# Optimization experiments

Measured on AMD Instinct MI355X. Metric: run time of the kernel, lower is better.

Reference implementation:

```python
import jax, jax.numpy as jnp
import numpy as np

N_HEADS = 32
N_KV_HEADS = 8
HEAD_DIM = 128
DIM = 4096
ROPE_THETA = 500000.0
BSZ, SEQLEN = 4, 1024


def _rope(t, cos, sin):
    # t: [B,S,H,hd]; cos/sin: [S,hd//2]
    te = t[..., 0::2]
    to = t[..., 1::2]
    c = cos[None, :, None, :]
    s = sin[None, :, None, :]
    out = jnp.stack([te * c - to * s, te * s + to * c], axis=-1)
    return out.reshape(t.shape)


def setup_inputs() -> dict:
    key = jax.random.key(0)
    ks = jax.random.split(key, 8)
    scale = 1.0 / np.sqrt(DIM)
    x = jax.random.normal(ks[0], (BSZ, SEQLEN, DIM), dtype=jnp.float32)
    wq = jax.random.normal(ks[1], (DIM, N_HEADS * HEAD_DIM), dtype=jnp.float32) * scale
    wk = jax.random.normal(ks[2], (DIM, N_KV_HEADS * HEAD_DIM), dtype=jnp.float32) * scale
    wv = jax.random.normal(ks[3], (DIM, N_KV_HEADS * HEAD_DIM), dtype=jnp.float32) * scale
    wo = jax.random.normal(ks[4], (N_HEADS * HEAD_DIM, DIM), dtype=jnp.float32) * scale
    # rotary tables: freqs_cis[s, j] = exp(i * s * theta^(-2j/hd))
    inv_freq = 1.0 / (ROPE_THETA ** (np.arange(0, HEAD_DIM, 2, dtype=np.float32) / HEAD_DIM))
    ang = np.outer(np.arange(SEQLEN, dtype=np.float32), inv_freq)
    freqs_cos = jnp.asarray(np.cos(ang), dtype=jnp.float32)
    freqs_sin = jnp.asarray(np.sin(ang), dtype=jnp.float32)
    # additive causal mask: 0 on/below diag, -inf above
    causal_mask = jnp.triu(jnp.full((SEQLEN, SEQLEN), -jnp.inf, dtype=jnp.float32), k=1)
    return {"x": x, "wq": wq, "wk": wk, "wv": wv, "wo": wo,
            "freqs_cos": freqs_cos, "freqs_sin": freqs_sin,
            "causal_mask": causal_mask, "fixed_point_iter": 0, "start_pos": 0}


def reference(x, wq, wk, wv, wo, freqs_cos, freqs_sin, causal_mask, fixed_point_iter, start_pos):
    B, S, _ = x.shape
    n_rep = N_HEADS // N_KV_HEADS
    xq = (x @ wq).reshape(B, S, N_HEADS, HEAD_DIM)
    xk = (x @ wk).reshape(B, S, N_KV_HEADS, HEAD_DIM)
    xv = (x @ wv).reshape(B, S, N_KV_HEADS, HEAD_DIM)
    xq = _rope(xq, freqs_cos, freqs_sin)
    xk = _rope(xk, freqs_cos, freqs_sin)
    # start_pos == 0 prefill: cache slice [:start_pos+S] equals freshly written xk/xv
    keys = jnp.repeat(xk, n_rep, axis=2)    # [B,S,H,hd]
    values = jnp.repeat(xv, n_rep, axis=2)
    scores = jnp.einsum('bqhd,bkhd->bhqk', xq, keys) / np.sqrt(HEAD_DIM)
    scores = scores + causal_mask  # broadcast [S,S]
    probs = jax.nn.softmax(scores.astype(jnp.float32), axis=-1).astype(xq.dtype)
    out = jnp.einsum('bhqk,bkhd->bqhd', probs, values)
    out = out.reshape(B, S, N_HEADS * HEAD_DIM)
    return out @ wo
```

## Files before the change

### kernel.cpp

```cpp
#include <hip/hip_runtime.h>

#define BSZ_  4
#define SEQ_  1024
#define NH_   32
#define NKVH_ 8
#define HD_   128
#define DIM_  4096
#define NTOK_ (BSZ_ * SEQ_)
#define QKVW_ 6144

typedef float  floatx4  __attribute__((ext_vector_type(4)));
typedef float  floatx16 __attribute__((ext_vector_type(16)));
typedef __bf16 bf16x8   __attribute__((ext_vector_type(8)));
typedef unsigned short ushortx8 __attribute__((ext_vector_type(8)));

__device__ __forceinline__ float fast_exp2(float x) {
  return __builtin_amdgcn_exp2f(x);
}

__device__ __forceinline__ unsigned short f2bf_bits(float f) {
  unsigned int u = __float_as_uint(f);
  u += 0x7FFFu + ((u >> 16) & 1u);
  return (unsigned short)(u >> 16);
}
__device__ __forceinline__ unsigned int pack_bf2_rne(float lo, float hi_) {
  return (unsigned int)f2bf_bits(lo) | ((unsigned int)f2bf_bits(hi_) << 16);
}
__device__ __forceinline__ unsigned int pack_bf2_trunc(float lo, float hi_) {
  return __builtin_amdgcn_perm(__float_as_uint(hi_), __float_as_uint(lo), 0x07060302u);
}

__device__ __forceinline__ void gld16(const void* g, void* l) {
  __builtin_amdgcn_global_load_lds(
      (const __attribute__((address_space(1))) void*)g,
      (__attribute__((address_space(3))) void*)l, 16, 0, 0);
}

__global__ __launch_bounds__(256)
void xconv(const float* __restrict__ X, unsigned short* __restrict__ XB)
{
  size_t i = ((size_t)blockIdx.x * 256 + threadIdx.x) * 4;
  float4 v = *(const float4*)&X[i];
  ushort4 o;
  o.x = f2bf_bits(v.x); o.y = f2bf_bits(v.y);
  o.z = f2bf_bits(v.z); o.w = f2bf_bits(v.w);
  *(ushort4*)&XB[i] = o;
}

__global__ __launch_bounds__(256)
void wtrans(const float* __restrict__ W, unsigned short* __restrict__ WT,
            int K, int N)
{
  __shared__ unsigned short T[32][36];
  const int k0 = blockIdx.y * 32, n0 = blockIdx.x * 32;
  const int t = threadIdx.x;
  {
    int kr = t >> 3, nc = (t & 7) * 4;
    float4 v = *(const float4*)&W[(size_t)(k0 + kr) * N + n0 + nc];
    T[kr][nc + 0] = f2bf_bits(v.x);
    T[kr][nc + 1] = f2bf_bits(v.y);
    T[kr][nc + 2] = f2bf_bits(v.z);
    T[kr][nc + 3] = f2bf_bits(v.w);
  }
  __syncthreads();
  {
    int nr = t >> 3, kc = (t & 7) * 4;
    ushort4 o;
    o.x = T[kc + 0][nr]; o.y = T[kc + 1][nr];
    o.z = T[kc + 2][nr]; o.w = T[kc + 3][nr];
    *(ushort4*)&WT[(size_t)(n0 + nr) * K + k0 + kc] = o;
  }
}

__global__ __launch_bounds__(256)
void vtrans2(const unsigned short* __restrict__ qkv, unsigned short* __restrict__ VT)
{
  __shared__ unsigned short T[32][36];
  const int bh = blockIdx.z;
  const int s0 = blockIdx.x * 32, d0 = blockIdx.y * 32;
  const int b = bh >> 3, kvh = bh & 7;
  const int t = threadIdx.x;
  {
    int sr = t >> 3, dc = (t & 7) * 4;
    ushort4 v = *(const ushort4*)&qkv[(size_t)(b * SEQ_ + s0 + sr) * QKVW_ + 5120 + kvh * HD_ + d0 + dc];
    T[sr][dc + 0] = v.x; T[sr][dc + 1] = v.y;
    T[sr][dc + 2] = v.z; T[sr][dc + 3] = v.w;
  }
  __syncthreads();
  {
    int dr = t >> 3, sc = (t & 7) * 4;
    ushort4 o;
    o.x = T[sc + 0][dr]; o.y = T[sc + 1][dr];
    o.z = T[sc + 2][dr]; o.w = T[sc + 3][dr];
    *(ushort4*)&VT[((size_t)bh * HD_ + d0 + dr) * SEQ_ + s0 + sc] = o;
  }
}

__global__ __launch_bounds__(256)
void rope2(unsigned int* __restrict__ t, const float* __restrict__ cosf,
           const float* __restrict__ sinf, int shift, int stride_u32, int base_u32)
{
  int idx = blockIdx.x * 256 + threadIdx.x;
  int tok = idx >> shift;
  int rem = idx & ((1 << shift) - 1);
  int d2  = idx & 63;
  int pos = tok & (SEQ_ - 1);
  unsigned int* p = &t[(size_t)tok * stride_u32 + base_u32 + rem];
  unsigned int pv = *p;
  float xe = __uint_as_float(pv << 16);
  float xo = __uint_as_float(pv & 0xFFFF0000u);
  float cv = cosf[pos * 64 + d2];
  float sv = sinf[pos * 64 + d2];
  float oe = xe * cv - xo * sv;
  float oo = xe * sv + xo * cv;
  *p = pack_bf2_rne(oe, oo);
}

template<bool OUT_BF16>
__global__ __launch_bounds__(512, 2)
void gemm_v4(const unsigned short* __restrict__ A,
             const unsigned short* __restrict__ B,
             void* __restrict__ Cout, int M, int N, int K)
{
  __shared__ __align__(16) unsigned short As[4][256][32];
  __shared__ __align__(16) unsigned short Bs[4][256][32];

  const int tid  = threadIdx.x;
  const int w    = tid >> 6;
  const int lane = tid & 63;
  const int l16  = lane & 15;
  const int quad = lane >> 4;
  const int wr   = w >> 2;
  const int wc   = w & 3;

  int wg = blockIdx.x;
  const int q8 = gridDim.x >> 3;
  wg = (wg & 7) * q8 + (wg >> 3);
  const int nbx = N >> 8;
  const int bm = (wg / nbx) * 256;
  const int bn = (wg % nbx) * 256;

  const int srow = w * 16 + (lane >> 2);
  const int scs  = (lane & 3) ^ ((srow >> 1) & 3);
  const unsigned short* Ag = &A[(size_t)(bm + srow) * K + scs * 8];
  const unsigned short* Bg = &B[(size_t)(bn + srow) * K + scs * 8];
  const size_t half = (size_t)128 * K;
  char* AsW = (char*)&As[0][0][0] + w * 1024;
  char* BsW = (char*)&Bs[0][0][0] + w * 1024;

  const int ntiles = K >> 5;

  auto stage = [&](int kt, int buf) {
    size_t ko = (size_t)kt << 5;
    gld16(Ag + ko,        AsW + buf * 16384);
    gld16(Ag + ko + half, AsW + buf * 16384 + 8192);
    gld16(Bg + ko,        BsW + buf * 16384);
    gld16(Bg + ko + half, BsW + buf * 16384 + 8192);
  };

  floatx4 acc[8][4];
#pragma unroll
  for (int i = 0; i < 8; i++)
#pragma unroll
    for (int j = 0; j < 4; j++) acc[i][j] = (floatx4){0.f, 0.f, 0.f, 0.f};

  const int cfr = quad ^ ((l16 >> 1) & 3);

  auto ldfrags = [&](int kt, bf16x8* aF, bf16x8* bF) {
    const int buf = kt & 3;
    const unsigned short* Ab = &As[buf][wr * 128 + l16][cfr * 8];
    const unsigned short* Bb = &Bs[buf][wc * 64  + l16][cfr * 8];
#pragma unroll
    for (int i = 0; i < 8; i++) aF[i] = *(const bf16x8*)&Ab[i * (16 * 32)];
#pragma unroll
    for (int j = 0; j < 4; j++) bF[j] = *(const bf16x8*)&Bb[j * (16 * 32)];
  };

  auto domfma = [&](bf16x8* aF, bf16x8* bF) {
    __builtin_amdgcn_s_setprio(1);
#pragma unroll
    for (int i = 0; i < 8; i++)
#pragma unroll
      for (int j = 0; j < 4; j++)
        acc[i][j] = __builtin_amdgcn_mfma_f32_16x16x32_bf16(aF[i], bF[j], acc[i][j], 0, 0, 0);
    __builtin_amdgcn_s_setprio(0);
  };

  auto syncstep = [&]() {
    asm volatile("s_waitcnt vmcnt(8)" ::: "memory");
    asm volatile("s_waitcnt lgkmcnt(0)" ::: "memory");
    __builtin_amdgcn_s_barrier();
    __builtin_amdgcn_sched_barrier(0);
  };

  bf16x8 aF0[8], bF0[4], aF1[8], bF1[4];

  stage(0, 0); stage(1, 1); stage(2, 2);
  syncstep();
  ldfrags(0, aF0, bF0);

#pragma unroll 1
  for (int t = 0; t < ntiles; t += 2) {
    {
      int pk = t + 3 < ntiles ? t + 3 : 0;
      stage(pk, (t + 3) & 3);
    }
    syncstep();
    ldfrags(t + 1, aF1, bF1);
    domfma(aF0, bF0);

    {
      int pk = t + 4 < ntiles ? t + 4 : 0;
      stage(pk, (t + 4) & 3);
    }
    syncstep();
    {
      int kt2 = t + 2 < ntiles ? t + 2 : 0;
      ldfrags(kt2, aF0, bF0);
    }
    domfma(aF1, bF1);
  }

  asm volatile("s_waitcnt vmcnt(0)" ::: "memory");

#pragma unroll
  for (int i = 0; i < 8; i++)
#pragma unroll
    for (int j = 0; j < 4; j++)
#pragma unroll
      for (int r = 0; r < 4; r++) {
        size_t row = bm + wr * 128 + i * 16 + quad * 4 + r;
        size_t col = bn + wc * 64 + j * 16 + l16;
        if (OUT_BF16)
          ((unsigned short*)Cout)[row * N + col] = f2bf_bits(acc[i][j][r]);
        else
          ((float*)Cout)[row * N + col] = acc[i][j][r];
      }
}

__global__ __launch_bounds__(256, 2)
void flash_attn2(const unsigned short* __restrict__ qkv,
                 const unsigned short* __restrict__ vt,
                 unsigned short* __restrict__ o)
{
  __shared__ __align__(16) unsigned short S_[4][8192];
  unsigned short* Ks = &S_[0][0];
  unsigned short* Vs = &S_[1][0];

  const int qt = blockIdx.x, h = blockIdx.y, b = blockIdx.z;
  const int kvh = h >> 2;
  const int tid = threadIdx.x, w = tid >> 6, lane = tid & 63;
  const int l31 = lane & 31, hi = lane >> 5;
  const int qb = qt * 256, qw = qb + w * 64;
  unsigned short* Ps = &S_[2][0] + w * 4096;

  const float CEXP = (float)(0.08838834764831845 * 1.4426950408889634);

  bf16x8 qf[2][8];
#pragma unroll
  for (int t2 = 0; t2 < 2; t2++) {
    const unsigned short* qrow =
        &qkv[(size_t)(b * SEQ_ + qw + t2 * 32 + l31) * QKVW_ + h * HD_ + hi * 8];
#pragma unroll
    for (int s = 0; s < 8; s++)
      qf[t2][s] = *(const bf16x8*)&qrow[s * 16];
  }

  floatx16 oa[2][4];
#pragma unroll
  for (int t2 = 0; t2 < 2; t2++)
#pragma unroll
    for (int dt = 0; dt < 4; dt++)
#pragma unroll
      for (int r = 0; r < 16; r++) oa[t2][dt][r] = 0.f;

  float ms[2] = {-3.0e38f, -3.0e38f};
  float ls[2] = {0.f, 0.f};

  const int nk = qb + 256;
  const int qmaxw = qw + 63;

  for (int kb_ = 0; kb_ < nk; kb_ += 64) {
    __syncthreads();
    {
      const size_t gbase = (size_t)(b * SEQ_ + kb_) * QKVW_ + 4096 + kvh * HD_;
#pragma unroll
      for (int it = 0; it < 4; it++) {
        int idx = it * 256 + tid;
        int key = idx >> 4, c = idx & 15;
        ushortx8 vld = *(const ushortx8*)&qkv[gbase + (size_t)key * QKVW_ + c * 8];
        *(ushortx8*)&Ks[key * 128 + ((c ^ (key & 15)) * 8)] = vld;
      }
      const size_t vbase = ((size_t)(b * NKVH_ + kvh) * HD_) * SEQ_ + kb_;
#pragma unroll
      for (int it = 0; it < 4; it++) {
        int idx = it * 256 + tid;
        int d = idx >> 3, c = idx & 7;
        ushortx8 vld = *(const ushortx8*)&vt[vbase + (size_t)d * SEQ_ + c * 8];
        *(ushortx8*)&Vs[d * 64 + ((c ^ (d & 7)) * 8)] = vld;
      }
    }
    __syncthreads();

    if (kb_ <= qmaxw) {
      const bool needmask = (kb_ + 63 > qw);

#pragma unroll
      for (int t2 = 0; t2 < 2; t2++) {
        floatx16 sc[2];
#pragma unroll
        for (int r = 0; r < 16; r++) { sc[0][r] = 0.f; sc[1][r] = 0.f; }
#pragma unroll
        for (int s = 0; s < 8; s++) {
          int c = 2 * s + hi;
          bf16x8 k0 = *(const bf16x8*)&Ks[l31 * 128 + ((c ^ (l31 & 15)) * 8)];
          bf16x8 k1 = *(const bf16x8*)&Ks[(32 + l31) * 128 + ((c ^ ((32 + l31) & 15)) * 8)];
          sc[0] = __builtin_amdgcn_mfma_f32_32x32x16_bf16(k0, qf[t2][s], sc[0], 0, 0, 0);
          sc[1] = __builtin_amdgcn_mfma_f32_32x32x16_bf16(k1, qf[t2][s], sc[1], 0, 0, 0);
        }

        if (needmask) {
          const int q = qw + t2 * 32 + l31;
#pragma unroll
          for (int k2 = 0; k2 < 2; k2++)
#pragma unroll
            for (int r = 0; r < 16; r++) {
              int key = kb_ + k2 * 32 + (r & 3) + 8 * (r >> 2) + 4 * hi;
              if (key > q) sc[k2][r] = -3.0e38f;
            }
        }

        float mx0 = sc[0][0], mx1 = sc[0][1];
#pragma unroll
        for (int r = 2; r < 16; r += 2) { mx0 = fmaxf(mx0, sc[0][r]); mx1 = fmaxf(mx1, sc[0][r + 1]); }
#pragma unroll
        for (int r = 0; r < 16; r += 2) { mx0 = fmaxf(mx0, sc[1][r]); mx1 = fmaxf(mx1, sc[1][r + 1]); }
        float mx = fmaxf(mx0, mx1);
        mx = fmaxf(mx, __shfl_xor(mx, 32));
        float mxs = mx * CEXP;
        float mn = fmaxf(ms[t2], mxs);
        float alpha = fast_exp2(ms[t2] - mn);
        ms[t2] = mn;

        float rs0 = 0.f, rs1 = 0.f;
        const int qloc = t2 * 32 + l31;
#pragma unroll
        for (int k2 = 0; k2 < 2; k2++) {
          unsigned int pk[8];
#pragma unroll
          for (int r = 0; r < 16; r += 2) {
            float p0 = fast_exp2(__builtin_fmaf(sc[k2][r],     CEXP, -mn));
            float p1 = fast_exp2(__builtin_fmaf(sc[k2][r + 1], CEXP, -mn));
            rs0 += p0; rs1 += p1;
            pk[r >> 1] = pack_bf2_trunc(p0, p1);
          }
#pragma unroll
          for (int rq = 0; rq < 4; rq++) {
            int keyoff = k2 * 32 + 8 * rq + 4 * hi;
            int c = keyoff >> 3;
            uint2 val = {pk[rq * 2], pk[rq * 2 + 1]};
            *(uint2*)&Ps[qloc * 64 + ((c ^ (qloc & 7)) * 8) + (keyoff & 7)] = val;
          }
        }
        float rs = rs0 + rs1;
        rs += __shfl_xor(rs, 32);
        ls[t2] = ls[t2] * alpha + rs;

        if (__any(alpha != 1.0f)) {
#pragma unroll
          for (int dt = 0; dt < 4; dt++)
#pragma unroll
            for (int r = 0; r < 16; r++) oa[t2][dt][r] *= alpha;
        }
      }

#pragma unroll
      for (int ks = 0; ks < 4; ks++) {
        int c = 2 * ks + hi;
        bf16x8 pf0, pf1;
        {
          int q0l = l31;
          int q1l = 32 + l31;
          pf0 = *(const bf16x8*)&Ps[q0l * 64 + ((c ^ (q0l & 7)) * 8)];
          pf1 = *(const bf16x8*)&Ps[q1l * 64 + ((c ^ (q1l & 7)) * 8)];
        }
#pragma unroll
        for (int dt = 0; dt < 4; dt++) {
          int d = dt * 32 + l31;
          bf16x8 vf = *(const bf16x8*)&Vs[d * 64 + ((c ^ (d & 7)) * 8)];
          oa[0][dt] = __builtin_amdgcn_mfma_f32_32x32x16_bf16(vf, pf0, oa[0][dt], 0, 0, 0);
          oa[1][dt] = __builtin_amdgcn_mfma_f32_32x32x16_bf16(vf, pf1, oa[1][dt], 0, 0, 0);
        }
      }
    }
  }

  __syncthreads();
  unsigned short* patch = &S_[w][0];
  float inv[2] = {1.0f / ls[0], 1.0f / ls[1]};
#pragma unroll
  for (int t2 = 0; t2 < 2; t2++) {
    const int qloc = t2 * 32 + l31;
#pragma unroll
    for (int dt = 0; dt < 4; dt++)
#pragma unroll
      for (int rq = 0; rq < 4; rq++) {
        float a0 = oa[t2][dt][rq * 4 + 0] * inv[t2];
        float a1 = oa[t2][dt][rq * 4 + 1] * inv[t2];
        float a2 = oa[t2][dt][rq * 4 + 2] * inv[t2];
        float a3 = oa[t2][dt][rq * 4 + 3] * inv[t2];
        int doff = dt * 32 + 8 * rq + 4 * hi;
        int c = doff >> 3;
        uint2 val = {pack_bf2_rne(a0, a1), pack_bf2_rne(a2, a3)};
        *(uint2*)&patch[qloc * 128 + ((c ^ (qloc & 7)) * 8) + (doff & 7)] = val;
      }
  }
#pragma unroll
  for (int it = 0; it < 16; it++) {
    int idx = it * 64 + lane;
    int row = idx >> 4, c = idx & 15;
    int cc = (c & 7) ^ (row & 7);
    int cs = (c & 8) | cc;
    ushortx8 vv = *(const ushortx8*)&patch[row * 128 + cs * 8];
    *(ushortx8*)&o[(size_t)(b * SEQ_ + qb + w * 64 + row) * 4096 + h * HD_ + c * 8] = vv;
  }
}

extern "C" void kernel_launch(void* const* d_in, const int* in_sizes, int n_in,
                              void* d_out, int out_size, void* d_ws, size_t ws_size,
                              hipStream_t stream)
{
  const float* x  = (const float*)d_in[0];
  const float* wq = (const float*)d_in[1];
  const float* wk = (const float*)d_in[2];
  const float* wv = (const float*)d_in[3];
  const float* wo = (const float*)d_in[4];
  const float* fc = (const float*)d_in[5];
  const float* fs = (const float*)d_in[6];
  float* out = (float*)d_out;

  unsigned short* xb    = (unsigned short*)d_ws;
  unsigned short* wqkvT = xb    + (size_t)NTOK_ * DIM_;
  unsigned short* qkvb  = wqkvT + (size_t)QKVW_ * DIM_;
  unsigned short* vtb   = qkvb  + (size_t)NTOK_ * QKVW_;
  unsigned short* ab    = xb;
  unsigned short* woT   = wqkvT;

  dim3 blk(256);

  xconv<<<(NTOK_ * DIM_ / 4) / 256, blk, 0, stream>>>(x, xb);
  wtrans<<<dim3(DIM_ / 32, DIM_ / 32), blk, 0, stream>>>(wq, wqkvT, DIM_, DIM_);
  wtrans<<<dim3((NKVH_ * HD_) / 32, DIM_ / 32), blk, 0, stream>>>(wk, wqkvT + (size_t)4096 * DIM_, DIM_, NKVH_ * HD_);
  wtrans<<<dim3((NKVH_ * HD_) / 32, DIM_ / 32), blk, 0, stream>>>(wv, wqkvT + (size_t)5120 * DIM_, DIM_, NKVH_ * HD_);

  gemm_v4<true><<<dim3((NTOK_ / 256) * (QKVW_ / 256)), dim3(512), 0, stream>>>(
      xb, wqkvT, qkvb, NTOK_, QKVW_, DIM_);

  wtrans<<<dim3(DIM_ / 32, DIM_ / 32), blk, 0, stream>>>(wo, woT, DIM_, DIM_);

  rope2<<<(NTOK_ * 2048) / 256, blk, 0, stream>>>((unsigned int*)qkvb, fc, fs, 11, 3072, 0);
  rope2<<<(NTOK_ * 512) / 256, blk, 0, stream>>>((unsigned int*)qkvb, fc, fs, 9, 3072, 2048);

  vtrans2<<<dim3(SEQ_ / 32, HD_ / 32, BSZ_ * NKVH_), blk, 0, stream>>>(qkvb, vtb);

  flash_attn2<<<dim3(SEQ_ / 256, NH_, BSZ_), blk, 0, stream>>>(qkvb, vtb, ab);

  gemm_v4<false><<<dim3((NTOK_ / 256) * (DIM_ / 256)), dim3(512), 0, stream>>>(
      ab, woT, out, NTOK_, DIM_, DIM_);
}
```

Before: 750.2 us.

## Restructure GEMM main loop into finer-grained interleaved load/MFMA pipeline

Replaces the 4-buffer, 2-tile-per-iteration GEMM pipeline with a 64-wide K-tile schedule that issues half-tile A/B global-to-LDS loads one at a time, each followed by a small LDS fragment read and a 16-MFMA burst. The finer interleaving is meant to overlap memory traffic with tensor math more evenly and to lower fragment register pressure (4 A fragments instead of 8 per set). In exchange it adds many more barriers per K step and a more delicate vmcnt accounting that must match the staged load order.

```diff
diff --git a/kernel.cpp b/kernel.cpp
--- a/kernel.cpp
+++ b/kernel.cpp
@@ -118,12 +118,12 @@
 
 template<bool OUT_BF16>
 __global__ __launch_bounds__(512, 2)
-void gemm_v4(const unsigned short* __restrict__ A,
+void gemm_v5(const unsigned short* __restrict__ A,
              const unsigned short* __restrict__ B,
              void* __restrict__ Cout, int M, int N, int K)
 {
-  __shared__ __align__(16) unsigned short As[4][256][32];
-  __shared__ __align__(16) unsigned short Bs[4][256][32];
+  __shared__ __align__(16) unsigned short As[2][2][256][32];
+  __shared__ __align__(16) unsigned short Bs[2][2][256][32];
 
   const int tid  = threadIdx.x;
   const int w    = tid >> 6;
@@ -145,17 +145,20 @@
   const unsigned short* Ag = &A[(size_t)(bm + srow) * K + scs * 8];
   const unsigned short* Bg = &B[(size_t)(bn + srow) * K + scs * 8];
   const size_t half = (size_t)128 * K;
-  char* AsW = (char*)&As[0][0][0] + w * 1024;
-  char* BsW = (char*)&Bs[0][0][0] + w * 1024;
-
-  const int ntiles = K >> 5;
-
-  auto stage = [&](int kt, int buf) {
-    size_t ko = (size_t)kt << 5;
-    gld16(Ag + ko,        AsW + buf * 16384);
-    gld16(Ag + ko + half, AsW + buf * 16384 + 8192);
-    gld16(Bg + ko,        BsW + buf * 16384);
-    gld16(Bg + ko + half, BsW + buf * 16384 + 8192);
+  char* AsB = (char*)&As[0][0][0][0];
+  char* BsB = (char*)&Bs[0][0][0][0];
+
+  auto stageA = [&](int kt, int d, int kk) {
+    size_t ko = (size_t)kt * 64 + (size_t)kk * 32;
+    char* dst = AsB + (d * 2 + kk) * 16384 + w * 1024;
+    gld16(Ag + ko,        dst);
+    gld16(Ag + ko + half, dst + 8192);
+  };
+  auto stageB = [&](int kt, int d, int kk) {
+    size_t ko = (size_t)kt * 64 + (size_t)kk * 32;
+    char* dst = BsB + (d * 2 + kk) * 16384 + w * 1024;
+    gld16(Bg + ko,        dst);
+    gld16(Bg + ko + half, dst + 8192);
   };
 
   floatx4 acc[8][4];
@@ -165,60 +168,58 @@
     for (int j = 0; j < 4; j++) acc[i][j] = (floatx4){0.f, 0.f, 0.f, 0.f};
 
   const int cfr = quad ^ ((l16 >> 1) & 3);
-
-  auto ldfrags = [&](int kt, bf16x8* aF, bf16x8* bF) {
-    const int buf = kt & 3;
-    const unsigned short* Ab = &As[buf][wr * 128 + l16][cfr * 8];
-    const unsigned short* Bb = &Bs[buf][wc * 64  + l16][cfr * 8];
-#pragma unroll
-    for (int i = 0; i < 8; i++) aF[i] = *(const bf16x8*)&Ab[i * (16 * 32)];
-#pragma unroll
-    for (int j = 0; j < 4; j++) bF[j] = *(const bf16x8*)&Bb[j * (16 * 32)];
-  };
-
-  auto domfma = [&](bf16x8* aF, bf16x8* bF) {
+  const unsigned short* ArF = &As[0][0][wr * 128 + l16][cfr * 8];
+  const unsigned short* BrF = &Bs[0][0][wc * 64  + l16][cfr * 8];
+
+  bf16x8 aF[4], bF[4];
+  auto rdA = [&](int d, int kk, int h) {
+    const unsigned short* p = ArF + (d * 2 + kk) * 8192 + h * 2048;
+#pragma unroll
+    for (int i = 0; i < 4; i++) aF[i] = *(const bf16x8*)&p[i * 512];
+  };
+  auto rdB = [&](int d, int kk) {
+    const unsigned short* p = BrF + (d * 2 + kk) * 8192;
+#pragma unroll
+    for (int j = 0; j < 4; j++) bF[j] = *(const bf16x8*)&p[j * 512];
+  };
+  auto mfma16 = [&](int h) {
     __builtin_amdgcn_s_setprio(1);
 #pragma unroll
-    for (int i = 0; i < 8; i++)
+    for (int i = 0; i < 4; i++)
 #pragma unroll
       for (int j = 0; j < 4; j++)
-        acc[i][j] = __builtin_amdgcn_mfma_f32_16x16x32_bf16(aF[i], bF[j], acc[i][j], 0, 0, 0);
+        acc[h * 4 + i][j] = __builtin_amdgcn_mfma_f32_16x16x32_bf16(aF[i], bF[j], acc[h * 4 + i][j], 0, 0, 0);
     __builtin_amdgcn_s_setprio(0);
   };
-
-  auto syncstep = [&]() {
-    asm volatile("s_waitcnt vmcnt(8)" ::: "memory");
+  auto vmc6 = [&]() { asm volatile("s_waitcnt vmcnt(6)" ::: "memory"); };
+  auto midsync = [&]() {
+    __builtin_amdgcn_s_barrier();
     asm volatile("s_waitcnt lgkmcnt(0)" ::: "memory");
-    __builtin_amdgcn_s_barrier();
     __builtin_amdgcn_sched_barrier(0);
   };
-
-  bf16x8 aF0[8], bF0[4], aF1[8], bF1[4];
-
-  stage(0, 0); stage(1, 1); stage(2, 2);
-  syncstep();
-  ldfrags(0, aF0, bF0);
+  auto endbar = [&]() { __builtin_amdgcn_s_barrier(); };
+
+  const int nt = K >> 6;
+
+  stageA(0, 0, 0); stageB(0, 0, 0); stageA(0, 0, 1); stageB(0, 0, 1); stageA(1, 1, 0);
+  asm volatile("s_waitcnt vmcnt(4)" ::: "memory");
+  __builtin_amdgcn_s_barrier();
 
 #pragma unroll 1
-  for (int t = 0; t < ntiles; t += 2) {
-    {
-      int pk = t + 3 < ntiles ? t + 3 : 0;
-      stage(pk, (t + 3) & 3);
-    }
-    syncstep();
-    ldfrags(t + 1, aF1, bF1);
-    domfma(aF0, bF0);
-
-    {
-      int pk = t + 4 < ntiles ? t + 4 : 0;
-      stage(pk, (t + 4) & 3);
-    }
-    syncstep();
-    {
-      int kt2 = t + 2 < ntiles ? t + 2 : 0;
-      ldfrags(kt2, aF0, bF0);
-    }
-    domfma(aF1, bF1);
+  for (int t = 0; t < nt; t += 2) {
+    const int k1 = t + 1;
+    const int k2 = (t + 2 < nt) ? t + 2 : 0;
+    const int k3 = (t + 3 < nt) ? t + 3 : 0;
+
+    stageB(k1, 1, 0); vmc6(); rdA(0, 0, 0); rdB(0, 0); midsync(); mfma16(0); endbar();
+    stageA(k1, 1, 1); vmc6(); rdA(0, 0, 1);            midsync(); mfma16(1); endbar();
+    stageB(k1, 1, 1); vmc6(); rdA(0, 1, 0); rdB(0, 1); midsync(); mfma16(0); endbar();
+    stageA(k2, 0, 0); vmc6(); rdA(0, 1, 1);            midsync(); mfma16(1); endbar();
+
+    stageB(k2, 0, 0); vmc6(); rdA(1, 0, 0); rdB(1, 0); midsync(); mfma16(0); endbar();
+    stageA(k2, 0, 1); vmc6(); rdA(1, 0, 1);            midsync(); mfma16(1); endbar();
+    stageB(k2, 0, 1); vmc6(); rdA(1, 1, 0); rdB(1, 1); midsync(); mfma16(0); endbar();
+    stageA(k3, 1, 0); vmc6(); rdA(1, 1, 1);            midsync(); mfma16(1); endbar();
   }
 
   asm volatile("s_waitcnt vmcnt(0)" ::: "memory");
@@ -453,7 +454,7 @@
   wtrans<<<dim3((NKVH_ * HD_) / 32, DIM_ / 32), blk, 0, stream>>>(wk, wqkvT + (size_t)4096 * DIM_, DIM_, NKVH_ * HD_);
   wtrans<<<dim3((NKVH_ * HD_) / 32, DIM_ / 32), blk, 0, stream>>>(wv, wqkvT + (size_t)5120 * DIM_, DIM_, NKVH_ * HD_);
 
-  gemm_v4<true><<<dim3((NTOK_ / 256) * (QKVW_ / 256)), dim3(512), 0, stream>>>(
+  gemm_v5<true><<<dim3((NTOK_ / 256) * (QKVW_ / 256)), dim3(512), 0, stream>>>(
       xb, wqkvT, qkvb, NTOK_, QKVW_, DIM_);
 
   wtrans<<<dim3(DIM_ / 32, DIM_ / 32), blk, 0, stream>>>(wo, woT, DIM_, DIM_);
@@ -465,6 +466,6 @@
 
   flash_attn2<<<dim3(SEQ_ / 256, NH_, BSZ_), blk, 0, stream>>>(qkvb, vtb, ab);
 
-  gemm_v4<false><<<dim3((NTOK_ / 256) * (DIM_ / 256)), dim3(512), 0, stream>>>(
+  gemm_v5<false><<<dim3((NTOK_ / 256) * (DIM_ / 256)), dim3(512), 0, stream>>>(
       ab, woT, out, NTOK_, DIM_, DIM_);
 }
```

New measurement: 777.6 us. 1.04x slower.
